# Kernel optimization log

Hardware: AMD Instinct MI355X
Metric: run time of the kernel (lower is better)

The kernel has to match this reference:

```python
import jax, jax.numpy as jnp
import numpy as np

D_MODEL = 1024
NEG_INF = -1e9


def setup_inputs() -> dict:
    key = jax.random.key(0)
    ks = jax.random.split(key, 9)
    B, S, D = 8, 2048, D_MODEL
    q = jax.random.normal(ks[0], (B, S, D), dtype=jnp.float32)
    k = jax.random.normal(ks[1], (B, S, D), dtype=jnp.float32)
    v = jax.random.normal(ks[2], (B, S, D), dtype=jnp.float32)
    mask = jax.random.randint(ks[3], (B, S), 0, 2, dtype=jnp.int32)
    scale = 1.0 / np.sqrt(D)
    Wq = jax.random.normal(ks[4], (D, D), dtype=jnp.float32) * scale
    bq = jnp.zeros((D,), dtype=jnp.float32)
    Wout = jax.random.normal(ks[5], (D, D), dtype=jnp.float32) * scale
    bout = jnp.zeros((D,), dtype=jnp.float32)
    return {"q": q, "k": k, "v": v, "mask": mask,
            "Wq": Wq, "bq": bq, "Wout": Wout, "bout": bout}


def reference(q, k, v, mask, Wq, bq, Wout, bout):
    # Faithful to original: the SAME q_linear projects q, k and v.
    qp = jnp.einsum('bsd,ed->bse', q, Wq) + bq
    kp = jnp.einsum('bsd,ed->bse', k, Wq) + bq
    vp = jnp.einsum('bsd,ed->bse', v, Wq) + bq
    d_k = q.shape[-1]
    # original divides K by sqrt(d_k) before the matmul (same math as scaling scores)
    scores = jnp.einsum('bqd,bkd->bqk', qp, kp) / jnp.sqrt(jnp.float32(d_k))  # [B,Sq,Sk]
    m = mask[:, None, :]  # [B,1,Sk]
    scores = jnp.where(m == 0, jnp.float32(-1e9), scores)
    weights = jax.nn.softmax(scores, axis=-1)
    out = jnp.einsum('bqk,bkd->bqd', weights, vp)
    out = jnp.einsum('bqd,ed->bqe', out, Wout) + bout
    return (out, weights)
```

## Files before the change

kernel.cpp:

```cpp
#include <hip/hip_runtime.h>
#include <hip/hip_bf16.h>

typedef __attribute__((ext_vector_type(8))) short short8;
typedef __attribute__((ext_vector_type(4))) float f32x4;

#define S_LEN 2048
#define DM 1024
#define NBATCH 8

__device__ __forceinline__ ushort f2b(float f) {
    union { float f; unsigned u; } a; a.f = f;
    unsigned u = a.u;
    u += 0x7fffu + ((u >> 16) & 1u);
    return (ushort)(u >> 16);
}

__device__ __forceinline__ float lo2f(unsigned p) {
    union { unsigned u; float f; } a; a.u = p << 16;
    return a.f;
}
__device__ __forceinline__ float hi2f(unsigned p) {
    union { unsigned u; float f; } a; a.u = p & 0xffff0000u;
    return a.f;
}

__device__ __forceinline__ unsigned pkbf(float a, float b) {
    float2 t; t.x = a; t.y = b;
    __hip_bfloat162 h = __float22bfloat162_rn(t);
    union { __hip_bfloat162 h; unsigned u; } c; c.h = h;
    return c.u;
}

#define GLDS(gp, lp) __builtin_amdgcn_global_load_lds( \
    (const __attribute__((address_space(1))) void*)(gp), \
    (__attribute__((address_space(3))) void*)(lp), 16, 0, 0)

#define BAR() __builtin_amdgcn_s_barrier()
#define VMW(N) asm volatile("s_waitcnt vmcnt(" #N ")" ::: "memory")

#define QUAD(AF, BF, MH, NH) do {                                              \
    __builtin_amdgcn_s_setprio(1);                                             \
    _Pragma("unroll") for (int m_ = 0; m_ < 4; m_++)                           \
    _Pragma("unroll") for (int n_ = 0; n_ < 2; n_++)                           \
    _Pragma("unroll") for (int ks_ = 0; ks_ < 2; ks_++)                        \
        acc[(MH)*4 + m_][(NH)*2 + n_] = __builtin_amdgcn_mfma_f32_16x16x32_bf16( \
            AF[m_][ks_], BF[n_][ks_], acc[(MH)*4 + m_][(NH)*2 + n_], 0, 0, 0); \
    __builtin_amdgcn_s_setprio(0);                                             \
} while (0)

template<int OMODE, bool HAS_BIAS>
__global__ __launch_bounds__(512, 2) void gemm256(
    const ushort* __restrict__ A, const ushort* __restrict__ B,
    void* __restrict__ Cv, const float* __restrict__ bias,
    int K, int lda, int ldb, int ldc,
    long long sA, long long sB, long long sC)
{
    __shared__ __align__(16) ushort lA[2][2][128 * 64];
    __shared__ __align__(16) ushort lB[2][2][128 * 64];

    const int t = threadIdx.x;
    const int lane = t & 63;
    const int wid = t >> 6;
    const int wm = wid >> 2, wn = wid & 3;
    const int z = blockIdx.z;

    const int gx = gridDim.x, gy = gridDim.y;
    const int nwg = gx * gy;
    const int lid = blockIdx.y * gx + blockIdx.x;
    const int qq = nwg >> 3, r8 = nwg & 7;
    const int xcd = lid & 7, off = lid >> 3;
    const int w = (xcd < r8 ? xcd * (qq + 1) : r8 * (qq + 1) + (xcd - r8) * qq) + off;
    const int bm = w / gy, bn = w % gy;

    const ushort* Ap = A + (size_t)z * sA + (size_t)(bm * 256) * lda;
    const ushort* Bp = B + (size_t)z * sB + (size_t)(bn * 256) * ldb;

    f32x4 acc[8][4] = {};

    const int srow = t >> 3;
    const int scol = ((t & 7) ^ (srow & 7)) * 8;

    auto stA = [&](int kt, int h, int buf) {
        const ushort* g = Ap + (size_t)(h * 128 + srow) * lda + kt * 64 + scol;
        char* d = (char*)lA[buf][h];
        GLDS(g, d + t * 16);
        GLDS(g + (size_t)64 * lda, d + 8192 + t * 16);
    };
    auto stB = [&](int kt, int h, int buf) {
        const ushort* g = Bp + (size_t)(h * 128 + srow) * ldb + kt * 64 + scol;
        char* d = (char*)lB[buf][h];
        GLDS(g, d + t * 16);
        GLDS(g + (size_t)64 * ldb, d + 8192 + t * 16);
    };

    const int nK = K >> 6;

    stA(0, 0, 0); stB(0, 0, 0); stA(0, 1, 0); stB(0, 1, 0);
    if (nK > 1) {
        stA(1, 0, 1); stB(1, 0, 1);
        VMW(4);
    } else {
        VMW(0);
    }
    BAR();

    const int r = lane & 15;
    const int swz = (r & 7) << 4;
    const int cb0 = ((lane >> 4) * 16) ^ swz;
    const int cb1 = (64 + (lane >> 4) * 16) ^ swz;
    const int lbr = (wn & 1) * 64;
    const int bh = wn >> 1;

    int cur = 0;
    for (int kt = 0; kt < nK; ++kt) {
        const char* la = (const char*)lA[cur][wm];
        const char* lb = (const char*)lB[cur][bh];
        short8 af[4][2], b0f[2][2], b1f[2][2];

#pragma unroll
        for (int m = 0; m < 4; m++) {
            const int lr = m * 16 + r;
            af[m][0] = *(const short8*)(la + lr * 128 + cb0);
            af[m][1] = *(const short8*)(la + lr * 128 + cb1);
        }
#pragma unroll
        for (int n = 0; n < 2; n++) {
            const int lr = lbr + n * 16 + r;
            b0f[n][0] = *(const short8*)(lb + lr * 128 + cb0);
            b0f[n][1] = *(const short8*)(lb + lr * 128 + cb1);
        }
        if (kt + 1 < nK) stA(kt + 1, 1, cur ^ 1);
        BAR();
        QUAD(af, b0f, 0, 0);
        BAR();

#pragma unroll
        for (int n = 0; n < 2; n++) {
            const int lr = lbr + 32 + n * 16 + r;
            b1f[n][0] = *(const short8*)(lb + lr * 128 + cb0);
            b1f[n][1] = *(const short8*)(lb + lr * 128 + cb1);
        }
        if (kt + 1 < nK) stB(kt + 1, 1, cur ^ 1);
        BAR();
        QUAD(af, b1f, 0, 1);
        BAR();

#pragma unroll
        for (int m = 0; m < 4; m++) {
            const int lr = 64 + m * 16 + r;
            af[m][0] = *(const short8*)(la + lr * 128 + cb0);
            af[m][1] = *(const short8*)(la + lr * 128 + cb1);
        }
        if (kt + 2 < nK) stB(kt + 2, 0, cur);
        BAR();
        QUAD(af, b0f, 1, 0);
        BAR();

        if (kt + 2 < nK) stA(kt + 2, 0, cur);
        BAR();
        QUAD(af, b1f, 1, 1);

        if (kt + 1 < nK) {
            if (kt + 1 == nK - 1) { VMW(0); } else { VMW(4); }
        }
        BAR();
        cur ^= 1;
    }

    const int ro = (lane >> 4) * 4;
    const int colb = bn * 256 + wn * 64;
    const int rowb = bm * 256 + wm * 128;
    float bv[4];
    if constexpr (HAS_BIAS) {
#pragma unroll
        for (int n = 0; n < 4; n++) bv[n] = bias[colb + n * 16 + r];
    }

    if constexpr (OMODE == 0) {
        float* Cp = (float*)Cv + (size_t)z * sC;
#pragma unroll
        for (int m = 0; m < 8; m++)
#pragma unroll
            for (int n = 0; n < 4; n++) {
                const int col = colb + n * 16 + r;
#pragma unroll
                for (int j = 0; j < 4; j++) {
                    float vv = acc[m][n][j];
                    if constexpr (HAS_BIAS) vv += bv[n];
                    Cp[(size_t)(rowb + m * 16 + ro + j) * ldc + col] = vv;
                }
            }
    } else if constexpr (OMODE == 1) {
        ushort* Cp = (ushort*)Cv + (size_t)z * sC;
#pragma unroll
        for (int m = 0; m < 8; m++)
#pragma unroll
            for (int n = 0; n < 4; n++) {
                const int col = colb + n * 16 + r;
#pragma unroll
                for (int j = 0; j < 4; j++) {
                    float vv = acc[m][n][j];
                    if constexpr (HAS_BIAS) vv += bv[n];
                    Cp[(size_t)(rowb + m * 16 + ro + j) * ldc + col] = f2b(vv);
                }
            }
    } else {
        ushort* Cp = (ushort*)Cv + (size_t)z * sC;
#pragma unroll
        for (int m = 0; m < 8; m++)
#pragma unroll
            for (int n = 0; n < 4; n++) {
                const int col = colb + n * 16 + r;
                float v0 = acc[m][n][0], v1 = acc[m][n][1], v2 = acc[m][n][2], v3 = acc[m][n][3];
                if constexpr (HAS_BIAS) { v0 += bv[n]; v1 += bv[n]; v2 += bv[n]; v3 += bv[n]; }
                ushort4 u;
                u.x = f2b(v0); u.y = f2b(v1); u.z = f2b(v2); u.w = f2b(v3);
                *(ushort4*)&Cp[(size_t)col * ldc + rowb + m * 16 + ro] = u;
            }
    }
}

__global__ __launch_bounds__(256) void cast_f32_bf16_k(
    const float* __restrict__ in, ushort* __restrict__ outp, int n)
{
    int idx = (blockIdx.x * 256 + threadIdx.x) * 4;
    if (idx >= n) return;
    float4 f = *(const float4*)&in[idx];
    uint2 u; u.x = pkbf(f.x, f.y); u.y = pkbf(f.z, f.w);
    *(uint2*)&outp[idx] = u;
}

__global__ __launch_bounds__(256) void cast3_k(
    const float* __restrict__ q, const float* __restrict__ k,
    const float* __restrict__ v, ushort* __restrict__ outp, int n_each)
{
    const float* src = (blockIdx.y == 0) ? q : (blockIdx.y == 1) ? k : v;
    ushort* dst = outp + (size_t)blockIdx.y * n_each;
    const int stride = gridDim.x * 256 * 4;
    for (int idx = (blockIdx.x * 256 + threadIdx.x) * 4; idx < n_each; idx += stride) {
        float4 f = *(const float4*)&src[idx];
        uint2 u; u.x = pkbf(f.x, f.y); u.y = pkbf(f.z, f.w);
        *(uint2*)&dst[idx] = u;
    }
}

__global__ __launch_bounds__(256) void softmax_rows(
    const ushort* __restrict__ sc, const int* __restrict__ mask,
    float* __restrict__ w, ushort* __restrict__ wb)
{
    __shared__ float red[8];
    const int rid = blockIdx.x;
    const int b = rid >> 11;
    const ushort* srow = sc + (size_t)rid * S_LEN;
    float* row = w + (size_t)rid * S_LEN;
    ushort* brow = wb + (size_t)rid * S_LEN;
    const int* mrow = mask + (size_t)b * S_LEN;
    const int t = threadIdx.x;
    const int wid = t >> 6, lane = t & 63;
    const float scale = 0.03125f;

    const int idx = t * 8;
    uint4 s4 = *(const uint4*)&srow[idx];
    int4 m0 = *(const int4*)&mrow[idx];
    int4 m1 = *(const int4*)&mrow[idx + 4];

    float x[8];
    x[0] = (m0.x == 0) ? -1.0e9f : lo2f(s4.x) * scale;
    x[1] = (m0.y == 0) ? -1.0e9f : hi2f(s4.x) * scale;
    x[2] = (m0.z == 0) ? -1.0e9f : lo2f(s4.y) * scale;
    x[3] = (m0.w == 0) ? -1.0e9f : hi2f(s4.y) * scale;
    x[4] = (m1.x == 0) ? -1.0e9f : lo2f(s4.z) * scale;
    x[5] = (m1.y == 0) ? -1.0e9f : hi2f(s4.z) * scale;
    x[6] = (m1.z == 0) ? -1.0e9f : lo2f(s4.w) * scale;
    x[7] = (m1.w == 0) ? -1.0e9f : hi2f(s4.w) * scale;

    float mx = fmaxf(fmaxf(fmaxf(x[0], x[1]), fmaxf(x[2], x[3])),
                     fmaxf(fmaxf(x[4], x[5]), fmaxf(x[6], x[7])));
#pragma unroll
    for (int off = 32; off; off >>= 1) mx = fmaxf(mx, __shfl_xor(mx, off));
    if (lane == 0) red[wid] = mx;
    __syncthreads();
    mx = fmaxf(fmaxf(red[0], red[1]), fmaxf(red[2], red[3]));

    float sum = 0.0f;
#pragma unroll
    for (int i = 0; i < 8; i++) { x[i] = __expf(x[i] - mx); sum += x[i]; }
#pragma unroll
    for (int off = 32; off; off >>= 1) sum += __shfl_xor(sum, off);
    if (lane == 0) red[4 + wid] = sum;
    __syncthreads();
    sum = red[4] + red[5] + red[6] + red[7];
    const float inv = 1.0f / sum;

    float4 o0, o1;
    o0.x = x[0] * inv; o0.y = x[1] * inv; o0.z = x[2] * inv; o0.w = x[3] * inv;
    o1.x = x[4] * inv; o1.y = x[5] * inv; o1.z = x[6] * inv; o1.w = x[7] * inv;
    *(float4*)&row[idx] = o0;
    *(float4*)&row[idx + 4] = o1;
    uint4 ub;
    ub.x = pkbf(o0.x, o0.y); ub.y = pkbf(o0.z, o0.w);
    ub.z = pkbf(o1.x, o1.y); ub.w = pkbf(o1.z, o1.w);
    *(uint4*)&brow[idx] = ub;
}

extern "C" void kernel_launch(void* const* d_in, const int* in_sizes, int n_in,
                              void* d_out, int out_size, void* d_ws, size_t ws_size,
                              hipStream_t stream)
{
    const float* q    = (const float*)d_in[0];
    const float* k    = (const float*)d_in[1];
    const float* v    = (const float*)d_in[2];
    const int*   mask = (const int*)d_in[3];
    const float* Wq   = (const float*)d_in[4];
    const float* bq   = (const float*)d_in[5];
    const float* Wout = (const float*)d_in[6];
    const float* bout = (const float*)d_in[7];

    float* out     = (float*)d_out;
    float* weights = out + (size_t)NBATCH * S_LEN * DM;

    const size_t NTOK = (size_t)NBATCH * S_LEN;

    ushort* qkvb = (ushort*)weights;
    ushort* qb = qkvb;
    ushort* kb = qb + NTOK * DM;
    ushort* vb = kb + NTOK * DM;
    ushort* wbf = (ushort*)d_out;

    ushort* qp    = (ushort*)d_ws;
    ushort* kp    = qp + NTOK * DM;
    ushort* vpT   = kp + NTOK * DM;
    ushort* attn  = qp;
    ushort* Wqb   = vpT + NTOK * DM;
    ushort* Woutb = Wqb + (size_t)DM * DM;
    ushort* scb   = Woutb + (size_t)DM * DM;

    dim3 blk(256, 1, 1);
    dim3 blk5(512, 1, 1);

    cast_f32_bf16_k<<<dim3(1024, 1, 1), blk, 0, stream>>>(Wq, Wqb, DM * DM);
    cast_f32_bf16_k<<<dim3(1024, 1, 1), blk, 0, stream>>>(Wout, Woutb, DM * DM);
    cast3_k<<<dim3(2048, 3, 1), blk, 0, stream>>>(q, k, v, qkvb, (int)(NTOK * DM));

    gemm256<1, true><<<dim3(64, 4, 1), blk5, 0, stream>>>(
        qb, Wqb, qp, bq, 1024, 1024, 1024, 1024, 0, 0, 0);
    gemm256<1, true><<<dim3(64, 4, 1), blk5, 0, stream>>>(
        kb, Wqb, kp, bq, 1024, 1024, 1024, 1024, 0, 0, 0);
    gemm256<2, true><<<dim3(8, 4, NBATCH), blk5, 0, stream>>>(
        vb, Wqb, vpT, bq, 1024, 1024, 1024, 2048,
        (long long)S_LEN * DM, 0, (long long)DM * S_LEN);

    gemm256<1, false><<<dim3(8, 8, NBATCH), blk5, 0, stream>>>(
        qp, kp, scb, nullptr, 1024, 1024, 1024, 2048,
        (long long)S_LEN * DM, (long long)S_LEN * DM, (long long)S_LEN * S_LEN);

    softmax_rows<<<dim3(NBATCH * S_LEN, 1, 1), blk, 0, stream>>>(scb, mask, weights, wbf);

    gemm256<1, false><<<dim3(8, 4, NBATCH), blk5, 0, stream>>>(
        wbf, vpT, attn, nullptr, 2048, 2048, 2048, 1024,
        (long long)S_LEN * S_LEN, (long long)DM * S_LEN, (long long)S_LEN * DM);

    gemm256<0, true><<<dim3(64, 4, 1), blk5, 0, stream>>>(
        attn, Woutb, out, bout, 1024, 1024, 1024, 1024, 0, 0, 0);
}
```

Baseline: 454.9 us.

## Fuse fp32-to-bf16 input cast into projection GEMM A-operand loads

Removes the standalone cast kernel for q/k/v. The projection GEMMs now load the fp32 activations into registers, convert them to bf16 and write them to LDS, with a reworked wait/barrier schedule. The q and k projections are merged into one launch using the z dimension. This avoids writing and re-reading the bf16 copies of q/k/v, about 200MB of traffic. In exchange the A operand goes through registers instead of direct global-to-LDS loads, which adds VGPR pressure and doubles A read bytes per tile.

New measurement: 762.4 us. 67.6% more time.

```diff
diff --git a/kernel.cpp b/kernel.cpp
--- a/kernel.cpp
+++ b/kernel.cpp
@@ -37,6 +37,8 @@
 
 #define BAR() __builtin_amdgcn_s_barrier()
 #define VMW(N) asm volatile("s_waitcnt vmcnt(" #N ")" ::: "memory")
+#define LGKM0() asm volatile("s_waitcnt lgkmcnt(0)" ::: "memory")
+#define SCHED0() __builtin_amdgcn_sched_barrier(0)
 
 #define QUAD(AF, BF, MH, NH) do {                                              \
     __builtin_amdgcn_s_setprio(1);                                             \
@@ -48,9 +50,10 @@
     __builtin_amdgcn_s_setprio(0);                                             \
 } while (0)
 
-template<int OMODE, bool HAS_BIAS>
+template<int AMODE, int OMODE, bool HAS_BIAS>
 __global__ __launch_bounds__(512, 2) void gemm256(
-    const ushort* __restrict__ A, const ushort* __restrict__ B,
+    const void* __restrict__ Av, const void* __restrict__ Av2,
+    const ushort* __restrict__ B,
     void* __restrict__ Cv, const float* __restrict__ bias,
     int K, int lda, int ldb, int ldc,
     long long sA, long long sB, long long sC)
@@ -72,7 +75,6 @@
     const int w = (xcd < r8 ? xcd * (qq + 1) : r8 * (qq + 1) + (xcd - r8) * qq) + off;
     const int bm = w / gy, bn = w % gy;
 
-    const ushort* Ap = A + (size_t)z * sA + (size_t)(bm * 256) * lda;
     const ushort* Bp = B + (size_t)z * sB + (size_t)(bn * 256) * ldb;
 
     f32x4 acc[8][4] = {};
@@ -80,12 +82,43 @@
     const int srow = t >> 3;
     const int scol = ((t & 7) ^ (srow & 7)) * 8;
 
+    const ushort* Ap16 = (AMODE == 0)
+        ? (const ushort*)Av + (size_t)z * sA + (size_t)(bm * 256) * lda : nullptr;
     auto stA = [&](int kt, int h, int buf) {
-        const ushort* g = Ap + (size_t)(h * 128 + srow) * lda + kt * 64 + scol;
+        const ushort* g = Ap16 + (size_t)(h * 128 + srow) * lda + kt * 64 + scol;
         char* d = (char*)lA[buf][h];
         GLDS(g, d + t * 16);
         GLDS(g + (size_t)64 * lda, d + 8192 + t * 16);
     };
+
+    const float* Ap32 = nullptr;
+    if constexpr (AMODE == 1) {
+        const float* base = (Av2 != nullptr && z == 1) ? (const float*)Av2
+                                                       : (const float*)Av;
+        Ap32 = base + (size_t)z * sA + (size_t)(bm * 256) * lda;
+    }
+    float4 ar[8];
+    auto aload = [&](int kt) {
+#pragma unroll
+        for (int i = 0; i < 4; i++) {
+            const float* g = Ap32 + (size_t)((i >> 1) * 128 + (i & 1) * 64 + srow) * lda
+                           + kt * 64 + scol;
+            ar[2 * i]     = *(const float4*)g;
+            ar[2 * i + 1] = *(const float4*)(g + 4);
+        }
+    };
+    auto awrite = [&](int buf) {
+#pragma unroll
+        for (int i = 0; i < 4; i++) {
+            uint4 wv;
+            wv.x = pkbf(ar[2 * i].x,     ar[2 * i].y);
+            wv.y = pkbf(ar[2 * i].z,     ar[2 * i].w);
+            wv.z = pkbf(ar[2 * i + 1].x, ar[2 * i + 1].y);
+            wv.w = pkbf(ar[2 * i + 1].z, ar[2 * i + 1].w);
+            *(uint4*)((char*)lA[buf][i >> 1] + (i & 1) * 8192 + t * 16) = wv;
+        }
+    };
+
     auto stB = [&](int kt, int h, int buf) {
         const ushort* g = Bp + (size_t)(h * 128 + srow) * ldb + kt * 64 + scol;
         char* d = (char*)lB[buf][h];
@@ -95,14 +128,25 @@
 
     const int nK = K >> 6;
 
-    stA(0, 0, 0); stB(0, 0, 0); stA(0, 1, 0); stB(0, 1, 0);
-    if (nK > 1) {
-        stA(1, 0, 1); stB(1, 0, 1);
-        VMW(4);
+    if constexpr (AMODE == 0) {
+        stA(0, 0, 0); stB(0, 0, 0); stA(0, 1, 0); stB(0, 1, 0);
+        if (nK > 1) {
+            stA(1, 0, 1); stB(1, 0, 1);
+            VMW(4);
+        } else {
+            VMW(0);
+        }
+        BAR();
     } else {
-        VMW(0);
+        aload(0);
+        SCHED0();
+        stB(0, 0, 0); stB(0, 1, 0);
+        if (nK > 1) { stB(1, 0, 1); VMW(2); } else { VMW(0); }
+        awrite(0);
+        LGKM0();
+        SCHED0();
+        BAR();
     }
-    BAR();
 
     const int r = lane & 15;
     const int swz = (r & 7) << 4;
@@ -129,7 +173,11 @@
             b0f[n][0] = *(const short8*)(lb + lr * 128 + cb0);
             b0f[n][1] = *(const short8*)(lb + lr * 128 + cb1);
         }
-        if (kt + 1 < nK) stA(kt + 1, 1, cur ^ 1);
+        if constexpr (AMODE == 0) {
+            if (kt + 1 < nK) stA(kt + 1, 1, cur ^ 1);
+        } else {
+            if (kt + 1 < nK) { aload(kt + 1); SCHED0(); }
+        }
         BAR();
         QUAD(af, b0f, 0, 0);
         BAR();
@@ -156,12 +204,27 @@
         QUAD(af, b0f, 1, 0);
         BAR();
 
-        if (kt + 2 < nK) stA(kt + 2, 0, cur);
+        if constexpr (AMODE == 0) {
+            if (kt + 2 < nK) stA(kt + 2, 0, cur);
+        } else {
+            if (kt + 1 < nK) {
+                if (kt + 2 < nK) { VMW(4); } else { VMW(2); }
+                awrite(cur ^ 1);
+            }
+        }
         BAR();
         QUAD(af, b1f, 1, 1);
 
-        if (kt + 1 < nK) {
-            if (kt + 1 == nK - 1) { VMW(0); } else { VMW(4); }
+        if constexpr (AMODE == 0) {
+            if (kt + 1 < nK) {
+                if (kt + 1 == nK - 1) { VMW(0); } else { VMW(4); }
+            }
+        } else {
+            if (kt + 1 < nK) {
+                if (kt + 2 < nK) { VMW(2); } else { VMW(0); }
+            }
+            LGKM0();
+            SCHED0();
         }
         BAR();
         cur ^= 1;
@@ -228,20 +291,6 @@
     float4 f = *(const float4*)&in[idx];
     uint2 u; u.x = pkbf(f.x, f.y); u.y = pkbf(f.z, f.w);
     *(uint2*)&outp[idx] = u;
-}
-
-__global__ __launch_bounds__(256) void cast3_k(
-    const float* __restrict__ q, const float* __restrict__ k,
-    const float* __restrict__ v, ushort* __restrict__ outp, int n_each)
-{
-    const float* src = (blockIdx.y == 0) ? q : (blockIdx.y == 1) ? k : v;
-    ushort* dst = outp + (size_t)blockIdx.y * n_each;
-    const int stride = gridDim.x * 256 * 4;
-    for (int idx = (blockIdx.x * 256 + threadIdx.x) * 4; idx < n_each; idx += stride) {
-        float4 f = *(const float4*)&src[idx];
-        uint2 u; u.x = pkbf(f.x, f.y); u.y = pkbf(f.z, f.w);
-        *(uint2*)&dst[idx] = u;
-    }
 }
 
 __global__ __launch_bounds__(256) void softmax_rows(
@@ -321,10 +370,6 @@
 
     const size_t NTOK = (size_t)NBATCH * S_LEN;
 
-    ushort* qkvb = (ushort*)weights;
-    ushort* qb = qkvb;
-    ushort* kb = qb + NTOK * DM;
-    ushort* vb = kb + NTOK * DM;
     ushort* wbf = (ushort*)d_out;
 
     ushort* qp    = (ushort*)d_ws;
@@ -340,26 +385,24 @@
 
     cast_f32_bf16_k<<<dim3(1024, 1, 1), blk, 0, stream>>>(Wq, Wqb, DM * DM);
     cast_f32_bf16_k<<<dim3(1024, 1, 1), blk, 0, stream>>>(Wout, Woutb, DM * DM);
-    cast3_k<<<dim3(2048, 3, 1), blk, 0, stream>>>(q, k, v, qkvb, (int)(NTOK * DM));
-
-    gemm256<1, true><<<dim3(64, 4, 1), blk5, 0, stream>>>(
-        qb, Wqb, qp, bq, 1024, 1024, 1024, 1024, 0, 0, 0);
-    gemm256<1, true><<<dim3(64, 4, 1), blk5, 0, stream>>>(
-        kb, Wqb, kp, bq, 1024, 1024, 1024, 1024, 0, 0, 0);
-    gemm256<2, true><<<dim3(8, 4, NBATCH), blk5, 0, stream>>>(
-        vb, Wqb, vpT, bq, 1024, 1024, 1024, 2048,
+
+    gemm256<1, 1, true><<<dim3(64, 4, 2), blk5, 0, stream>>>(
+        q, k, Wqb, qp, bq, 1024, 1024, 1024, 1024,
+        0, 0, (long long)NTOK * DM);
+    gemm256<1, 2, true><<<dim3(8, 4, NBATCH), blk5, 0, stream>>>(
+        v, nullptr, Wqb, vpT, bq, 1024, 1024, 1024, 2048,
         (long long)S_LEN * DM, 0, (long long)DM * S_LEN);
 
-    gemm256<1, false><<<dim3(8, 8, NBATCH), blk5, 0, stream>>>(
-        qp, kp, scb, nullptr, 1024, 1024, 1024, 2048,
+    gemm256<0, 1, false><<<dim3(8, 8, NBATCH), blk5, 0, stream>>>(
+        qp, nullptr, kp, scb, nullptr, 1024, 1024, 1024, 2048,
         (long long)S_LEN * DM, (long long)S_LEN * DM, (long long)S_LEN * S_LEN);
 
     softmax_rows<<<dim3(NBATCH * S_LEN, 1, 1), blk, 0, stream>>>(scb, mask, weights, wbf);
 
-    gemm256<1, false><<<dim3(8, 4, NBATCH), blk5, 0, stream>>>(
-        wbf, vpT, attn, nullptr, 2048, 2048, 2048, 1024,
+    gemm256<0, 1, false><<<dim3(8, 4, NBATCH), blk5, 0, stream>>>(
+        wbf, nullptr, vpT, attn, nullptr, 2048, 2048, 2048, 1024,
         (long long)S_LEN * S_LEN, (long long)DM * S_LEN, (long long)S_LEN * DM);
 
-    gemm256<0, true><<<dim3(64, 4, 1), blk5, 0, stream>>>(
-        attn, Woutb, out, bout, 1024, 1024, 1024, 1024, 0, 0, 0);
-}
+    gemm256<0, 0, true><<<dim3(64, 4, 1), blk5, 0, stream>>>(
+        attn, nullptr, Woutb, out, bout, 1024, 1024, 1024, 1024, 0, 0, 0);
+}
```
